# Performance work log

Measured on AMD Instinct MI355X. Metric: run time of the kernel, lower is better.

## Reference

```python
import jax, jax.numpy as jnp
import numpy as np

EPS = 1e-5


def setup_inputs() -> dict:
    key = jax.random.key(0)
    k_x, k_y, k_w, k_b = jax.random.split(key, 4)
    B, IN, OUT = 16384, 1024, 1024
    x = jax.random.normal(k_x, (B, IN), dtype=jnp.float32)
    y = jax.random.normal(k_y, (B, OUT), dtype=jnp.float32)
    # nn.Linear default init scale ~ 1/sqrt(in_features); keep activations sane
    weight = jax.random.normal(k_w, (OUT, IN), dtype=jnp.float32) / np.sqrt(IN)
    bias = jax.random.normal(k_b, (OUT,), dtype=jnp.float32) / np.sqrt(IN)
    gamma = jnp.ones((OUT,), dtype=jnp.float32)
    beta = jnp.zeros((OUT,), dtype=jnp.float32)
    return {"x": x, "y": y, "weight": weight, "bias": bias, "gamma": gamma, "beta": beta}


def reference(x, y, weight, bias, gamma, beta):
    # Linear: z[b, o] = sum_i x[b, i] * weight[o, i] + bias[o]
    z = jnp.einsum('bi,oi->bo', x, weight) + bias
    # LayerNorm over the feature (out_features) dim, biased variance
    mean = jnp.mean(z, axis=-1, keepdims=True)
    var = jnp.mean(jnp.square(z), axis=-1, keepdims=True) - jnp.square(mean)
    ln = (z - mean) * jax.lax.rsqrt(var + EPS) * gamma + beta
    # residual add then elementwise multiply
    return (ln + y) * y
```

## Files before the change

kernel.cpp:

```cpp
#include <hip/hip_runtime.h>
#include <stdint.h>

typedef unsigned short u16;
typedef __attribute__((ext_vector_type(8))) short short8;
typedef __attribute__((ext_vector_type(4))) float floatx4;
typedef __attribute__((ext_vector_type(2))) float floatx2;

#define K_DIM 1024
#define N_DIM 1024
#define BK 32
#define NCHUNK 32
#define GCH 2
#define NGRP (NCHUNK / GCH)
#define BM 64
#define HCHUNK 16

__device__ __forceinline__ u16 f2b(float f) {
    union { float f; uint32_t i; } v; v.f = f;
    uint32_t u = v.i;
    return (u16)((u + 0x7FFFu + ((u >> 16) & 1u)) >> 16);
}
__device__ __forceinline__ float b2f(u16 u) {
    union { uint32_t i; float f; } v; v.i = ((uint32_t)u) << 16; return v.f;
}

__global__ __launch_bounds__(256) void pack_w_kernel(const float* __restrict__ w,
                                                     u16* __restrict__ wpk) {
    int gid  = blockIdx.x * 256 + threadIdx.x;
    int lane = gid & 63;
    int kc   = (gid >> 6) & 31;
    int tile = gid >> 11;
    int n = tile * 16 + (lane & 15);
    int k = kc * 32 + (lane >> 4) * 8;
    const float* src = w + (size_t)n * K_DIM + k;
    floatx4 a = *(const floatx4*)(src);
    floatx4 b = *(const floatx4*)(src + 4);
    short8 o;
    o[0] = (short)f2b(a[0]); o[1] = (short)f2b(a[1]);
    o[2] = (short)f2b(a[2]); o[3] = (short)f2b(a[3]);
    o[4] = (short)f2b(b[0]); o[5] = (short)f2b(b[1]);
    o[6] = (short)f2b(b[2]); o[7] = (short)f2b(b[3]);
    *(short8*)(wpk + (size_t)gid * 8) = o;
}

__global__ __launch_bounds__(512) void gemm256_kernel(
    const float* __restrict__ x, const u16* __restrict__ wpk,
    const float* __restrict__ bias, u16* __restrict__ zout,
    float* __restrict__ gsum, float* __restrict__ gsum2)
{
    __shared__ __align__(16) u16 smem[65536];
    __shared__ float ls_sum[256];
    __shared__ float ls_sum2[256];

    const int tid  = threadIdx.x;
    const int lane = tid & 63;
    const int wv   = tid >> 6;
    const int wr   = wv >> 1;
    const int wc   = wv & 1;
    const int q    = lane >> 4;
    const int rb   = blockIdx.x >> 2;
    const int cb   = blockIdx.x & 3;
    const int row0 = rb * 256;
    const int col0 = cb * 256;

    if (tid < 256) { ls_sum[tid] = 0.0f; ls_sum2[tid] = 0.0f; }

    const int rb8 = tid >> 4;
    const int sk  = (tid & 15) << 1;
    const int s_qs  = (sk >> 3) ^ ((rb8 >> 1) & 3);
    const int s_off0 = rb8 * 64 + s_qs * 16 + (sk & 7) * 2;
    const int s_off1 = s_off0 + 2048;
    const float* xb = x + (size_t)(row0 + rb8) * K_DIM + sk;

    const u16* wb0 = wpk + ((size_t)(cb * 16 + wv * 2) * 32) * 512 + lane * 8;
    const u16* wb1 = wpk + ((size_t)(cb * 16 + wv * 2 + 1) * 32) * 512 + lane * 8;

    const int a_base = (lane & 15) * 64 + (q ^ (((lane & 15) >> 1) & 3)) * 16;

    floatx4 acc[4][8];
#pragma unroll
    for (int mi = 0; mi < 4; ++mi)
#pragma unroll
        for (int ni = 0; ni < 8; ++ni)
            acc[mi][ni] = (floatx4){0.0f, 0.0f, 0.0f, 0.0f};

    {
        char* A0 = (char*)smem;
        char* B0 = (char*)smem + 65536;
#pragma unroll
        for (int c2 = 0; c2 < GCH; ++c2) {
#pragma unroll
            for (int j = 0; j < 8; ++j) {
                floatx2 v = *(const floatx2*)(xb + (size_t)((j & 1) * 32 + (j >> 1) * 64) * K_DIM + c2 * BK);
                uint32_t p = (uint32_t)f2b(v[0]) | ((uint32_t)f2b(v[1]) << 16);
                *(uint32_t*)(A0 + c2 * 16384 + (j >> 1) * 4096 + ((j & 1) ? s_off1 : s_off0)) = p;
            }
            short8 t0 = *(const short8*)(wb0 + (size_t)c2 * 512);
            short8 t1 = *(const short8*)(wb1 + (size_t)c2 * 512);
            *(short8*)(B0 + c2 * 16384 + (wv * 2) * 1024 + lane * 16)     = t0;
            *(short8*)(B0 + c2 * 16384 + (wv * 2 + 1) * 1024 + lane * 16) = t1;
        }
    }
    __syncthreads();

    floatx2 va[GCH][8];
    short8  bs[GCH][2];

#pragma unroll 1
    for (int g = 0; g < NGRP; ++g) {
        const int cur = g & 1;
        const int nxt = cur ^ 1;
        const bool pf = (g + 1 < NGRP);

        if (pf) {
            const int kb = (g + 1) * GCH;
#pragma unroll
            for (int c2 = 0; c2 < GCH; ++c2) {
#pragma unroll
                for (int j = 0; j < 8; ++j)
                    va[c2][j] = *(const floatx2*)(xb + (size_t)((j & 1) * 32 + (j >> 1) * 64) * K_DIM + (kb + c2) * BK);
                bs[c2][0] = *(const short8*)(wb0 + (size_t)(kb + c2) * 512);
                bs[c2][1] = *(const short8*)(wb1 + (size_t)(kb + c2) * 512);
            }
        }

#pragma unroll
        for (int c2 = 0; c2 < GCH; ++c2) {
            const char* Ab = (const char*)smem + cur * 32768 + c2 * 16384;
            const char* Bb = (const char*)smem + 65536 + cur * 32768 + c2 * 16384;
            short8 af[4];
#pragma unroll
            for (int mi = 0; mi < 4; ++mi)
                af[mi] = *(const short8*)(Ab + wr * 4096 + a_base + mi * 1024);
            short8 bf[8];
#pragma unroll
            for (int ni = 0; ni < 8; ++ni)
                bf[ni] = *(const short8*)(Bb + (wc * 8 + ni) * 1024 + lane * 16);
#pragma unroll
            for (int mi = 0; mi < 4; ++mi)
#pragma unroll
                for (int ni = 0; ni < 8; ++ni)
                    acc[mi][ni] = __builtin_amdgcn_mfma_f32_16x16x32_bf16(
                        af[mi], bf[ni], acc[mi][ni], 0, 0, 0);
        }

        if (pf) {
            char* An = (char*)smem + nxt * 32768;
            char* Bn = (char*)smem + 65536 + nxt * 32768;
#pragma unroll
            for (int c2 = 0; c2 < GCH; ++c2) {
#pragma unroll
                for (int j = 0; j < 8; ++j) {
                    uint32_t p = (uint32_t)f2b(va[c2][j][0]) | ((uint32_t)f2b(va[c2][j][1]) << 16);
                    *(uint32_t*)(An + c2 * 16384 + (j >> 1) * 4096 + ((j & 1) ? s_off1 : s_off0)) = p;
                }
                *(short8*)(Bn + c2 * 16384 + (wv * 2) * 1024 + lane * 16)     = bs[c2][0];
                *(short8*)(Bn + c2 * 16384 + (wv * 2 + 1) * 1024 + lane * 16) = bs[c2][1];
            }
        }

        asm volatile("s_waitcnt lgkmcnt(0)" ::: "memory");
        __builtin_amdgcn_s_barrier();
        asm volatile("" ::: "memory");
    }

    float bias_v[8];
#pragma unroll
    for (int ni = 0; ni < 8; ++ni)
        bias_v[ni] = bias[col0 + wc * 128 + ni * 16 + (lane & 15)];
#pragma unroll
    for (int mi = 0; mi < 4; ++mi)
#pragma unroll
        for (int ni = 0; ni < 8; ++ni)
#pragma unroll
            for (int r = 0; r < 4; ++r)
                acc[mi][ni][r] += bias_v[ni];

#pragma unroll
    for (int mi = 0; mi < 4; ++mi)
#pragma unroll
        for (int r = 0; r < 4; ++r) {
            float s = 0.0f, s2 = 0.0f;
#pragma unroll
            for (int ni = 0; ni < 8; ++ni) {
                float v = acc[mi][ni][r];
                s += v; s2 += v * v;
            }
#pragma unroll
            for (int m = 1; m < 16; m <<= 1) {
                s  += __shfl_xor(s,  m, 64);
                s2 += __shfl_xor(s2, m, 64);
            }
            if ((lane & 15) == 0) {
                int rl = wr * 64 + mi * 16 + (q << 2) + r;
                atomicAdd(&ls_sum[rl], s);
                atomicAdd(&ls_sum2[rl], s2);
            }
        }

    __syncthreads();
    if (tid < 256) {
        atomicAdd(&gsum[row0 + tid],  ls_sum[tid]);
        atomicAdd(&gsum2[row0 + tid], ls_sum2[tid]);
    }

    char* zb = (char*)smem;
    for (int s4 = 0; s4 < 4; ++s4) {
        if (wr == s4) {
#pragma unroll
            for (int mi = 0; mi < 4; ++mi)
#pragma unroll
                for (int ni = 0; ni < 8; ++ni)
#pragma unroll
                    for (int r = 0; r < 4; ++r) {
                        int lr  = mi * 16 + (q << 2) + r;
                        int col = wc * 128 + ni * 16 + (lane & 15);
                        int phys = lr * 512 + ((col << 1) ^ (q << 5));
                        *(u16*)(zb + phys) = f2b(acc[mi][ni][r]);
                    }
        }
        __syncthreads();
#pragma unroll
        for (int it = 0; it < 4; ++it) {
            int row = tid >> 3;
            int c8  = (tid & 7) + it * 8;
            int phys = row * 512 + ((c8 << 4) ^ (((row >> 2) & 3) << 5));
            short8 z8 = *(const short8*)(zb + phys);
            *(short8*)(zout + (size_t)(row0 + s4 * 64 + row) * N_DIM + col0 + c8 * 8) = z8;
        }
        __syncthreads();
    }
}

__global__ __launch_bounds__(256) void ln_apply_kernel(
    const u16* __restrict__ z, const float* __restrict__ y,
    const float* __restrict__ stats, const float* __restrict__ gamma,
    const float* __restrict__ beta, float* __restrict__ out)
{
    int g   = blockIdx.x * 256 + threadIdx.x;
    int row = g >> 7;
    int c8  = g & 127;
    float s  = stats[row];
    float s2 = stats[16384 + row];
    float mean = s * (1.0f / 1024.0f);
    float var  = s2 * (1.0f / 1024.0f) - mean * mean;
    float rs   = rsqrtf(var + 1e-5f);
    short8 z8 = *(const short8*)(z + (size_t)row * N_DIM + c8 * 8);
    const float* yp  = y     + (size_t)row * N_DIM + c8 * 8;
    const float* gp  = gamma + c8 * 8;
    const float* bpv = beta  + c8 * 8;
    float*       op  = out   + (size_t)row * N_DIM + c8 * 8;
    floatx4 y0 = *(const floatx4*)(yp);
    floatx4 y1 = *(const floatx4*)(yp + 4);
    floatx4 g0 = *(const floatx4*)(gp);
    floatx4 g1 = *(const floatx4*)(gp + 4);
    floatx4 b0 = *(const floatx4*)(bpv);
    floatx4 b1 = *(const floatx4*)(bpv + 4);
    floatx4 o0, o1;
#pragma unroll
    for (int e = 0; e < 4; ++e) {
        float zv = b2f((u16)z8[e]);
        o0[e] = ((zv - mean) * rs * g0[e] + b0[e] + y0[e]) * y0[e];
    }
#pragma unroll
    for (int e = 0; e < 4; ++e) {
        float zv = b2f((u16)z8[e + 4]);
        o1[e] = ((zv - mean) * rs * g1[e] + b1[e] + y1[e]) * y1[e];
    }
    *(floatx4*)(op)     = o0;
    *(floatx4*)(op + 4) = o1;
}

__global__ __launch_bounds__(1024) void fused_gemm_ln_kernel(
    const float* __restrict__ x, const float* __restrict__ y,
    const u16* __restrict__ wpk, const float* __restrict__ bias,
    const float* __restrict__ gamma, const float* __restrict__ beta,
    float* __restrict__ out)
{
    __shared__ __align__(16) u16 lds16[HCHUNK * BM * BK];
    __shared__ __align__(16) u16 zbuf[16 * 1024];
    __shared__ float ls_sum[64];
    __shared__ float ls_sum2[64];
    __shared__ float ls_mean[64];
    __shared__ float ls_rs[64];

    const int tid  = threadIdx.x;
    const int lane = tid & 63;
    const int wv   = tid >> 6;
    const int q    = lane >> 4;
    const int row0 = blockIdx.x * BM;

    if (tid < 64) { ls_sum[tid] = 0.0f; ls_sum2[tid] = 0.0f; }

    const int sr = tid >> 4;
    const int sk = (tid & 15) << 1;
    const float* s_src = x + (size_t)(row0 + sr) * K_DIM + sk;
    const int s_qs  = (sk >> 3) ^ ((sr >> 1) & 3);
    const int s_off = sr * 64 + s_qs * 16 + (sk & 7) * 2;

    const u16* bp = wpk + (size_t)wv * 65536 + lane * 8;
    const int a_base = (lane & 15) * 64 + (q ^ (((lane & 15) >> 1) & 3)) * 16;

    floatx4 acc[4][4];
#pragma unroll
    for (int mi = 0; mi < 4; ++mi)
#pragma unroll
        for (int ni = 0; ni < 4; ++ni)
            acc[mi][ni] = (floatx4){0.0f, 0.0f, 0.0f, 0.0f};

#pragma unroll 4
    for (int c = 0; c < HCHUNK; ++c) {
        floatx2 v = *(const floatx2*)(s_src + c * BK);
        uint32_t p = (uint32_t)f2b(v[0]) | ((uint32_t)f2b(v[1]) << 16);
        *(uint32_t*)((char*)lds16 + c * 4096 + s_off) = p;
    }
    short8 bfr[2][4];
#pragma unroll
    for (int ni = 0; ni < 4; ++ni)
        bfr[0][ni] = *(const short8*)(bp + ni * 16384);
    __syncthreads();

    for (int half = 0; half < 2; ++half) {
        if (half == 1) {
            __syncthreads();
#pragma unroll 4
            for (int c = 0; c < HCHUNK; ++c) {
                floatx2 v = *(const floatx2*)(s_src + (HCHUNK + c) * BK);
                uint32_t p = (uint32_t)f2b(v[0]) | ((uint32_t)f2b(v[1]) << 16);
                *(uint32_t*)((char*)lds16 + c * 4096 + s_off) = p;
            }
            __syncthreads();
        }
#pragma unroll 2
        for (int c = 0; c < HCHUNK; ++c) {
            const int kc  = half * HCHUNK + c;
            const int cur = kc & 1;
            const int nxt = cur ^ 1;
            const char* ab = (const char*)lds16 + c * 4096;
            short8 af0 = *(const short8*)(ab + a_base);
            short8 af1 = *(const short8*)(ab + a_base + 1024);
            short8 af2 = *(const short8*)(ab + a_base + 2048);
            short8 af3 = *(const short8*)(ab + a_base + 3072);
            const int kn = (kc + 1 < NCHUNK) ? (kc + 1) : kc;
#pragma unroll
            for (int ni = 0; ni < 4; ++ni)
                bfr[nxt][ni] = *(const short8*)(bp + ni * 16384 + kn * 512);
#pragma unroll
            for (int ni = 0; ni < 4; ++ni) {
                acc[0][ni] = __builtin_amdgcn_mfma_f32_16x16x32_bf16(af0, bfr[cur][ni], acc[0][ni], 0, 0, 0);
                acc[1][ni] = __builtin_amdgcn_mfma_f32_16x16x32_bf16(af1, bfr[cur][ni], acc[1][ni], 0, 0, 0);
                acc[2][ni] = __builtin_amdgcn_mfma_f32_16x16x32_bf16(af2, bfr[cur][ni], acc[2][ni], 0, 0, 0);
                acc[3][ni] = __builtin_amdgcn_mfma_f32_16x16x32_bf16(af3, bfr[cur][ni], acc[3][ni], 0, 0, 0);
            }
        }
    }

    float bias_v[4];
#pragma unroll
    for (int ni = 0; ni < 4; ++ni)
        bias_v[ni] = bias[(wv << 6) + (ni << 4) + (lane & 15)];
#pragma unroll
    for (int mi = 0; mi < 4; ++mi)
#pragma unroll
        for (int ni = 0; ni < 4; ++ni)
#pragma unroll
            for (int r = 0; r < 4; ++r)
                acc[mi][ni][r] += bias_v[ni];

    __syncthreads();

#pragma unroll
    for (int mi = 0; mi < 4; ++mi)
#pragma unroll
        for (int r = 0; r < 4; ++r) {
            float s = 0.0f, s2 = 0.0f;
#pragma unroll
            for (int ni = 0; ni < 4; ++ni) {
                float v = acc[mi][ni][r];
                s += v; s2 += v * v;
            }
#pragma unroll
            for (int m = 1; m < 16; m <<= 1) {
                s  += __shfl_xor(s,  m, 64);
                s2 += __shfl_xor(s2, m, 64);
            }
            if ((lane & 15) == 0) {
                int rl = (mi << 4) + (q << 2) + r;
                atomicAdd(&ls_sum[rl], s);
                atomicAdd(&ls_sum2[rl], s2);
            }
        }

    __syncthreads();
    if (tid < 64) {
        float mean = ls_sum[tid] * (1.0f / 1024.0f);
        float var  = ls_sum2[tid] * (1.0f / 1024.0f) - mean * mean;
        ls_mean[tid] = mean;
        ls_rs[tid]   = rsqrtf(var + 1e-5f);
    }

    for (int mi = 0; mi < 4; ++mi) {
#pragma unroll
        for (int ni = 0; ni < 4; ++ni)
#pragma unroll
            for (int r = 0; r < 4; ++r) {
                int lr   = (q << 2) + r;
                int lin  = (((wv << 6) + (ni << 4) + (lane & 15)) << 1);
                int phys = lr * 2048 + (lin ^ (q << 5));
                *(u16*)((char*)zbuf + phys) = f2b(acc[mi][ni][r]);
            }
        __syncthreads();
#pragma unroll
        for (int it = 0; it < 2; ++it) {
            int row  = (tid >> 7) + (it << 3);
            int c8   = tid & 127;
            int phys = row * 2048 + ((c8 << 4) ^ (((row >> 2) & 3) << 5));
            short8 z8 = *(const short8*)((const char*)zbuf + phys);
            int grow  = row0 + (mi << 4) + row;
            float mean = ls_mean[(mi << 4) + row];
            float rs   = ls_rs[(mi << 4) + row];
            const float* yp = y     + (size_t)grow * N_DIM + c8 * 8;
            const float* gp = gamma + c8 * 8;
            const float* bpv = beta + c8 * 8;
            float*       op = out   + (size_t)grow * N_DIM + c8 * 8;
            floatx4 y0 = *(const floatx4*)(yp);
            floatx4 y1 = *(const floatx4*)(yp + 4);
            floatx4 g0 = *(const floatx4*)(gp);
            floatx4 g1 = *(const floatx4*)(gp + 4);
            floatx4 b0 = *(const floatx4*)(bpv);
            floatx4 b1 = *(const floatx4*)(bpv + 4);
            floatx4 o0, o1;
#pragma unroll
            for (int e = 0; e < 4; ++e) {
                float zv = b2f((u16)z8[e]);
                o0[e] = ((zv - mean) * rs * g0[e] + b0[e] + y0[e]) * y0[e];
            }
#pragma unroll
            for (int e = 0; e < 4; ++e) {
                float zv = b2f((u16)z8[e + 4]);
                o1[e] = ((zv - mean) * rs * g1[e] + b1[e] + y1[e]) * y1[e];
            }
            *(floatx4*)(op)     = o0;
            *(floatx4*)(op + 4) = o1;
        }
        __syncthreads();
    }
}

extern "C" void kernel_launch(void* const* d_in, const int* in_sizes, int n_in,
                              void* d_out, int out_size, void* d_ws, size_t ws_size,
                              hipStream_t stream) {
    const float* x     = (const float*)d_in[0];
    const float* y     = (const float*)d_in[1];
    const float* wgt   = (const float*)d_in[2];
    const float* bias  = (const float*)d_in[3];
    const float* gamma = (const float*)d_in[4];
    const float* beta  = (const float*)d_in[5];
    float* out = (float*)d_out;

    u16* wpk = (u16*)d_ws;
    const size_t WPK_BYTES   = 2u * 1024u * 1024u;
    const size_t STATS_BYTES = 128u * 1024u;
    const size_t Z_BYTES     = 32u * 1024u * 1024u;
    const int M = in_sizes[0] / K_DIM;

    pack_w_kernel<<<512, 256, 0, stream>>>(wgt, wpk);

    if (ws_size >= WPK_BYTES + STATS_BYTES + Z_BYTES) {
        float* stats = (float*)((char*)d_ws + WPK_BYTES);
        u16*   zws   = (u16*)((char*)d_ws + WPK_BYTES + STATS_BYTES);
        hipMemsetAsync(stats, 0, STATS_BYTES, stream);
        gemm256_kernel<<<(M / 256) * 4, 512, 0, stream>>>(
            x, wpk, bias, zws, stats, stats + 16384);
        ln_apply_kernel<<<M * (N_DIM / 8) / 256, 256, 0, stream>>>(
            zws, y, stats, gamma, beta, out);
    } else {
        fused_gemm_ln_kernel<<<M / BM, 1024, 0, stream>>>(
            x, y, wpk, bias, gamma, beta, out);
    }
}
```

Before: 226.9 us.

## Restructure GEMM to 1024 threads with triple-buffered single-chunk LDS pipeline

Rewrites the 256x256 GEMM tile kernel to use 16 waves per block (4x4 wave grid) instead of 8. The K loop now handles one chunk per iteration with a three-slot LDS ring and a prefetch distance of two, where it previously ran two chunks per iteration through a double buffer. The A tile is stored in the MFMA fragment layout so each thread loads 8 contiguous floats. Block order is changed so that consecutive blocks share a column block of W. The aim is more latency hiding, wider loads and fewer registers per thread, at the cost of one barrier per chunk and fewer MFMAs per barrier.

```diff
diff --git a/kernel.cpp b/kernel.cpp
--- a/kernel.cpp
+++ b/kernel.cpp
@@ -10,8 +10,6 @@
 #define N_DIM 1024
 #define BK 32
 #define NCHUNK 32
-#define GCH 2
-#define NGRP (NCHUNK / GCH)
 #define BM 64
 #define HCHUNK 16
 
@@ -43,120 +41,91 @@
     *(short8*)(wpk + (size_t)gid * 8) = o;
 }
 
-__global__ __launch_bounds__(512) void gemm256_kernel(
+__global__ __launch_bounds__(1024) void gemm256v2_kernel(
     const float* __restrict__ x, const u16* __restrict__ wpk,
     const float* __restrict__ bias, u16* __restrict__ zout,
     float* __restrict__ gsum, float* __restrict__ gsum2)
 {
-    __shared__ __align__(16) u16 smem[65536];
+    __shared__ __align__(16) char smem[3 * 32768];
     __shared__ float ls_sum[256];
     __shared__ float ls_sum2[256];
 
     const int tid  = threadIdx.x;
     const int lane = tid & 63;
     const int wv   = tid >> 6;
-    const int wr   = wv >> 1;
-    const int wc   = wv & 1;
+    const int wr   = wv >> 2;
+    const int wc   = wv & 3;
     const int q    = lane >> 4;
-    const int rb   = blockIdx.x >> 2;
-    const int cb   = blockIdx.x & 3;
+    const int rb   = blockIdx.x & 63;
+    const int cb   = blockIdx.x >> 6;
     const int row0 = rb * 256;
     const int col0 = cb * 256;
 
     if (tid < 256) { ls_sum[tid] = 0.0f; ls_sum2[tid] = 0.0f; }
 
-    const int rb8 = tid >> 4;
-    const int sk  = (tid & 15) << 1;
-    const int s_qs  = (sk >> 3) ^ ((rb8 >> 1) & 3);
-    const int s_off0 = rb8 * 64 + s_qs * 16 + (sk & 7) * 2;
-    const int s_off1 = s_off0 + 2048;
-    const float* xb = x + (size_t)(row0 + rb8) * K_DIM + sk;
-
-    const u16* wb0 = wpk + ((size_t)(cb * 16 + wv * 2) * 32) * 512 + lane * 8;
-    const u16* wb1 = wpk + ((size_t)(cb * 16 + wv * 2 + 1) * 32) * 512 + lane * 8;
-
-    const int a_base = (lane & 15) * 64 + (q ^ (((lane & 15) >> 1) & 3)) * 16;
-
-    floatx4 acc[4][8];
-#pragma unroll
-    for (int mi = 0; mi < 4; ++mi)
-#pragma unroll
-        for (int ni = 0; ni < 8; ++ni)
+    const float* xb = x + (size_t)(row0 + (tid >> 2)) * K_DIM + ((tid & 3) << 3);
+    const int a_st = wv * 1024 + ((((tid >> 2) & 15) + (tid & 3) * 16) << 4);
+    const u16* wb = wpk + ((size_t)(cb * 16 + wv) * 32) * 512 + lane * 8;
+    const int b_st = 16384 + wv * 1024 + (lane << 4);
+
+    floatx4 acc[4][4];
+#pragma unroll
+    for (int mi = 0; mi < 4; ++mi)
+#pragma unroll
+        for (int ni = 0; ni < 4; ++ni)
             acc[mi][ni] = (floatx4){0.0f, 0.0f, 0.0f, 0.0f};
 
-    {
-        char* A0 = (char*)smem;
-        char* B0 = (char*)smem + 65536;
-#pragma unroll
-        for (int c2 = 0; c2 < GCH; ++c2) {
-#pragma unroll
-            for (int j = 0; j < 8; ++j) {
-                floatx2 v = *(const floatx2*)(xb + (size_t)((j & 1) * 32 + (j >> 1) * 64) * K_DIM + c2 * BK);
-                uint32_t p = (uint32_t)f2b(v[0]) | ((uint32_t)f2b(v[1]) << 16);
-                *(uint32_t*)(A0 + c2 * 16384 + (j >> 1) * 4096 + ((j & 1) ? s_off1 : s_off0)) = p;
-            }
-            short8 t0 = *(const short8*)(wb0 + (size_t)c2 * 512);
-            short8 t1 = *(const short8*)(wb1 + (size_t)c2 * 512);
-            *(short8*)(B0 + c2 * 16384 + (wv * 2) * 1024 + lane * 16)     = t0;
-            *(short8*)(B0 + c2 * 16384 + (wv * 2 + 1) * 1024 + lane * 16) = t1;
-        }
+#pragma unroll
+    for (int c = 0; c < 2; ++c) {
+        floatx4 a0 = *(const floatx4*)(xb + c * BK);
+        floatx4 a1 = *(const floatx4*)(xb + c * BK + 4);
+        short8 bv  = *(const short8*)(wb + (size_t)c * 512);
+        short8 aw;
+        aw[0] = (short)f2b(a0[0]); aw[1] = (short)f2b(a0[1]);
+        aw[2] = (short)f2b(a0[2]); aw[3] = (short)f2b(a0[3]);
+        aw[4] = (short)f2b(a1[0]); aw[5] = (short)f2b(a1[1]);
+        aw[6] = (short)f2b(a1[2]); aw[7] = (short)f2b(a1[3]);
+        *(short8*)(smem + c * 32768 + a_st) = aw;
+        *(short8*)(smem + c * 32768 + b_st) = bv;
     }
     __syncthreads();
 
-    floatx2 va[GCH][8];
-    short8  bs[GCH][2];
-
 #pragma unroll 1
-    for (int g = 0; g < NGRP; ++g) {
-        const int cur = g & 1;
-        const int nxt = cur ^ 1;
-        const bool pf = (g + 1 < NGRP);
-
+    for (int kc = 0; kc < NCHUNK; ++kc) {
+        const int slot_c = kc % 3;
+        const int slot_w = (kc + 2) % 3;
+        const bool pf = (kc + 2 < NCHUNK);
+
+        floatx4 a0, a1; short8 bv;
         if (pf) {
-            const int kb = (g + 1) * GCH;
-#pragma unroll
-            for (int c2 = 0; c2 < GCH; ++c2) {
-#pragma unroll
-                for (int j = 0; j < 8; ++j)
-                    va[c2][j] = *(const floatx2*)(xb + (size_t)((j & 1) * 32 + (j >> 1) * 64) * K_DIM + (kb + c2) * BK);
-                bs[c2][0] = *(const short8*)(wb0 + (size_t)(kb + c2) * 512);
-                bs[c2][1] = *(const short8*)(wb1 + (size_t)(kb + c2) * 512);
-            }
-        }
-
-#pragma unroll
-        for (int c2 = 0; c2 < GCH; ++c2) {
-            const char* Ab = (const char*)smem + cur * 32768 + c2 * 16384;
-            const char* Bb = (const char*)smem + 65536 + cur * 32768 + c2 * 16384;
-            short8 af[4];
-#pragma unroll
-            for (int mi = 0; mi < 4; ++mi)
-                af[mi] = *(const short8*)(Ab + wr * 4096 + a_base + mi * 1024);
-            short8 bf[8];
-#pragma unroll
-            for (int ni = 0; ni < 8; ++ni)
-                bf[ni] = *(const short8*)(Bb + (wc * 8 + ni) * 1024 + lane * 16);
-#pragma unroll
-            for (int mi = 0; mi < 4; ++mi)
-#pragma unroll
-                for (int ni = 0; ni < 8; ++ni)
-                    acc[mi][ni] = __builtin_amdgcn_mfma_f32_16x16x32_bf16(
-                        af[mi], bf[ni], acc[mi][ni], 0, 0, 0);
-        }
+            a0 = *(const floatx4*)(xb + (kc + 2) * BK);
+            a1 = *(const floatx4*)(xb + (kc + 2) * BK + 4);
+            bv = *(const short8*)(wb + (size_t)(kc + 2) * 512);
+        }
+
+        const char* As = smem + slot_c * 32768;
+        short8 af[4], bf[4];
+#pragma unroll
+        for (int mi = 0; mi < 4; ++mi)
+            af[mi] = *(const short8*)(As + (wr * 4 + mi) * 1024 + (lane << 4));
+#pragma unroll
+        for (int ni = 0; ni < 4; ++ni)
+            bf[ni] = *(const short8*)(As + 16384 + (wc * 4 + ni) * 1024 + (lane << 4));
+#pragma unroll
+        for (int mi = 0; mi < 4; ++mi)
+#pragma unroll
+            for (int ni = 0; ni < 4; ++ni)
+                acc[mi][ni] = __builtin_amdgcn_mfma_f32_16x16x32_bf16(
+                    af[mi], bf[ni], acc[mi][ni], 0, 0, 0);
 
         if (pf) {
-            char* An = (char*)smem + nxt * 32768;
-            char* Bn = (char*)smem + 65536 + nxt * 32768;
-#pragma unroll
-            for (int c2 = 0; c2 < GCH; ++c2) {
-#pragma unroll
-                for (int j = 0; j < 8; ++j) {
-                    uint32_t p = (uint32_t)f2b(va[c2][j][0]) | ((uint32_t)f2b(va[c2][j][1]) << 16);
-                    *(uint32_t*)(An + c2 * 16384 + (j >> 1) * 4096 + ((j & 1) ? s_off1 : s_off0)) = p;
-                }
-                *(short8*)(Bn + c2 * 16384 + (wv * 2) * 1024 + lane * 16)     = bs[c2][0];
-                *(short8*)(Bn + c2 * 16384 + (wv * 2 + 1) * 1024 + lane * 16) = bs[c2][1];
-            }
+            short8 aw;
+            aw[0] = (short)f2b(a0[0]); aw[1] = (short)f2b(a0[1]);
+            aw[2] = (short)f2b(a0[2]); aw[3] = (short)f2b(a0[3]);
+            aw[4] = (short)f2b(a1[0]); aw[5] = (short)f2b(a1[1]);
+            aw[6] = (short)f2b(a1[2]); aw[7] = (short)f2b(a1[3]);
+            *(short8*)(smem + slot_w * 32768 + a_st) = aw;
+            *(short8*)(smem + slot_w * 32768 + b_st) = bv;
         }
 
         asm volatile("s_waitcnt lgkmcnt(0)" ::: "memory");
@@ -164,14 +133,14 @@
         asm volatile("" ::: "memory");
     }
 
-    float bias_v[8];
-#pragma unroll
-    for (int ni = 0; ni < 8; ++ni)
-        bias_v[ni] = bias[col0 + wc * 128 + ni * 16 + (lane & 15)];
-#pragma unroll
-    for (int mi = 0; mi < 4; ++mi)
-#pragma unroll
-        for (int ni = 0; ni < 8; ++ni)
+    float bias_v[4];
+#pragma unroll
+    for (int ni = 0; ni < 4; ++ni)
+        bias_v[ni] = bias[col0 + wc * 64 + ni * 16 + (lane & 15)];
+#pragma unroll
+    for (int mi = 0; mi < 4; ++mi)
+#pragma unroll
+        for (int ni = 0; ni < 4; ++ni)
 #pragma unroll
             for (int r = 0; r < 4; ++r)
                 acc[mi][ni][r] += bias_v[ni];
@@ -182,7 +151,7 @@
         for (int r = 0; r < 4; ++r) {
             float s = 0.0f, s2 = 0.0f;
 #pragma unroll
-            for (int ni = 0; ni < 8; ++ni) {
+            for (int ni = 0; ni < 4; ++ni) {
                 float v = acc[mi][ni][r];
                 s += v; s2 += v * v;
             }
@@ -204,26 +173,26 @@
         atomicAdd(&gsum2[row0 + tid], ls_sum2[tid]);
     }
 
-    char* zb = (char*)smem;
+    char* zb = smem;
     for (int s4 = 0; s4 < 4; ++s4) {
         if (wr == s4) {
 #pragma unroll
             for (int mi = 0; mi < 4; ++mi)
 #pragma unroll
-                for (int ni = 0; ni < 8; ++ni)
+                for (int ni = 0; ni < 4; ++ni)
 #pragma unroll
                     for (int r = 0; r < 4; ++r) {
                         int lr  = mi * 16 + (q << 2) + r;
-                        int col = wc * 128 + ni * 16 + (lane & 15);
+                        int col = wc * 64 + ni * 16 + (lane & 15);
                         int phys = lr * 512 + ((col << 1) ^ (q << 5));
                         *(u16*)(zb + phys) = f2b(acc[mi][ni][r]);
                     }
         }
         __syncthreads();
 #pragma unroll
-        for (int it = 0; it < 4; ++it) {
-            int row = tid >> 3;
-            int c8  = (tid & 7) + it * 8;
+        for (int it = 0; it < 2; ++it) {
+            int row = tid >> 4;
+            int c8  = (tid & 15) + it * 16;
             int phys = row * 512 + ((c8 << 4) ^ (((row >> 2) & 3) << 5));
             short8 z8 = *(const short8*)(zb + phys);
             *(short8*)(zout + (size_t)(row0 + s4 * 64 + row) * N_DIM + col0 + c8 * 8) = z8;
@@ -470,7 +439,7 @@
         float* stats = (float*)((char*)d_ws + WPK_BYTES);
         u16*   zws   = (u16*)((char*)d_ws + WPK_BYTES + STATS_BYTES);
         hipMemsetAsync(stats, 0, STATS_BYTES, stream);
-        gemm256_kernel<<<(M / 256) * 4, 512, 0, stream>>>(
+        gemm256v2_kernel<<<(M / 256) * 4, 1024, 0, stream>>>(
             x, wpk, bias, zws, stats, stats + 16384);
         ln_apply_kernel<<<M * (N_DIM / 8) / 256, 256, 0, stream>>>(
             zws, y, stats, gamma, beta, out);
```

New measurement: 231.2 us. No clear change (+1.9%).
